# Performance work log

Measured on AMD Instinct MI355X. Metric: run time of the kernel, lower is better.

The kernel has to match this reference:

```python
import jax, jax.numpy as jnp
import numpy as np

HID = 128  # args['hidden_size']


def preprocess_adj(A):
    # A: [B, N, N] -> D^{-1/2} (A + I) D^{-1/2}
    N = A.shape[1]
    A_hat = A + jnp.eye(N, dtype=A.dtype)
    d = jnp.sum(A_hat, axis=2)                     # [B, N]
    d_safe = jnp.where(d > 0, d, 1.0)
    d_inv = jnp.where(d > 0, d_safe ** -0.5, 0.0)  # inf -> 0, as in torch code
    return d_inv[:, :, None] * A_hat * d_inv[:, None, :]


def lstm(x, w_ih, w_hh, b_ih, b_hh):
    # x: [B, T, H]; PyTorch gate order i, f, g, o; zero init state
    B = x.shape[0]
    H = w_hh.shape[1]
    def step(carry, xt):
        h, c = carry
        z = xt @ w_ih.T + b_ih + h @ w_hh.T + b_hh
        i, f, g, o = jnp.split(z, 4, axis=-1)
        c = jax.nn.sigmoid(f) * c + jax.nn.sigmoid(i) * jnp.tanh(g)
        h = jax.nn.sigmoid(o) * jnp.tanh(c)
        return (h, c), h
    h0 = jnp.zeros((B, H), x.dtype)
    c0 = jnp.zeros((B, H), x.dtype)
    _, hs = jax.lax.scan(step, (h0, c0), jnp.swapaxes(x, 0, 1))
    return jnp.swapaxes(hs, 0, 1)  # [B, T, H]


def gcn_dynamic_forward(x, A_norm, conv_w, conv_b, w_ih, w_hh, b_ih, b_hh):
    # x: [B, N, HID] with N >= HID: take last HID rows as dynamic-filter input
    df_in = x[:, x.shape[1] - HID:, :]              # [B, HID, HID]
    dyn = jax.lax.conv_general_dilated(
        df_in, conv_w, window_strides=(1,), padding=[(1, 1)],
        dimension_numbers=('NCH', 'OIH', 'NCH')) + conv_b[None, :, None]
    lw = lstm(dyn, w_ih, w_hh, b_ih, b_hh)          # [B, HID, HID]
    agg = jnp.matmul(A_norm, x)                     # [B, N, HID]
    out = jax.nn.sigmoid(jnp.matmul(agg, lw))       # output activation (1-layer GCN)
    return out                                       # dropout is identity in eval


def setup_inputs() -> dict:
    key = jax.random.key(0)
    ks = jax.random.split(key, 8)
    B, N = 4, 4096
    node_embedding = jax.random.normal(ks[0], (B, N, HID), dtype=jnp.float32)
    # sparse symmetric-ish 0/1 adjacency, avg degree ~ N*0.01
    adjacency_matrix = (jax.random.uniform(ks[1], (B, N, N)) < 0.01).astype(jnp.float32)
    s = 0.05
    conv_w = jax.random.normal(ks[2], (HID, HID, 3), dtype=jnp.float32) * s
    conv_b = jax.random.normal(ks[3], (HID,), dtype=jnp.float32) * s
    w_ih = jax.random.normal(ks[4], (4 * HID, HID), dtype=jnp.float32) * s
    w_hh = jax.random.normal(ks[5], (4 * HID, HID), dtype=jnp.float32) * s
    b_ih = jax.random.normal(ks[6], (4 * HID,), dtype=jnp.float32) * s
    b_hh = jax.random.normal(ks[7], (4 * HID,), dtype=jnp.float32) * s
    return {"node_embedding": node_embedding, "adjacency_matrix": adjacency_matrix,
            "conv_w": conv_w, "conv_b": conv_b,
            "w_ih": w_ih, "w_hh": w_hh, "b_ih": b_ih, "b_hh": b_hh}


def reference(node_embedding, adjacency_matrix, conv_w, conv_b, w_ih, w_hh, b_ih, b_hh):
    A_norm = preprocess_adj(adjacency_matrix)
    return gcn_dynamic_forward(node_embedding, A_norm, conv_w, conv_b, w_ih, w_hh, b_ih, b_hh)
```

## Files before the change

### kernel.cpp

```cpp
#include <hip/hip_runtime.h>
#include <hip/hip_cooperative_groups.h>
#include <math.h>

namespace cg = cooperative_groups;

#define N_NODES 4096
#define HIDN 128
#define MAXNZ 128
#define CGRID 512
#define NTHR 512

typedef float v4f __attribute__((ext_vector_type(4)));
typedef _Float16 h2 __attribute__((ext_vector_type(2)));
typedef _Float16 h8 __attribute__((ext_vector_type(8)));

__device__ __forceinline__ float fsig(float x) { return 1.0f / (1.0f + __expf(-x)); }
__device__ __forceinline__ float ftanh_(float x) { return 1.0f - 2.0f / (__expf(2.0f * x) + 1.0f); }


__device__ __forceinline__ void convz_body(
        int cb, int tid, const float* __restrict__ x,
        const float* __restrict__ conv_w, const float* __restrict__ conv_b,
        const float* __restrict__ w_ih, const float* __restrict__ b_ih,
        const float* __restrict__ b_hh, float* __restrict__ z3,
        float* dl ) {
    const int b = cb >> 5;
    const int t0 = (cb & 31) * 4;
    const int tsub = tid >> 7;
    const int h = tid & 127;
    const int t = t0 + tsub;
    {
        const float* xb = x + ((size_t)b * N_NODES + (N_NODES - HIDN)) * HIDN;
        const float* w = conv_w + (size_t)t * HIDN * 3;
        float a0 = conv_b[t], a1 = 0.0f, a2 = 0.0f, a3 = 0.0f;
        #pragma unroll 4
        for (int i = 0; i < HIDN; i += 4) {
            const float* xr0 = xb + (size_t)i * HIDN;
            #pragma unroll
            for (int s = 0; s < 4; ++s) {
                const float* xr = xr0 + s * HIDN;
                float w0 = w[(i + s) * 3 + 0], w1 = w[(i + s) * 3 + 1], w2 = w[(i + s) * 3 + 2];
                float left  = (h > 0)   ? xr[h - 1] : 0.0f;
                float mid   = xr[h];
                float right = (h < 127) ? xr[h + 1] : 0.0f;
                if (s == 0)      a0 += left * w0 + mid * w1 + right * w2;
                else if (s == 1) a1 += left * w0 + mid * w1 + right * w2;
                else if (s == 2) a2 += left * w0 + mid * w1 + right * w2;
                else             a3 += left * w0 + mid * w1 + right * w2;
            }
        }
        dl[tsub * HIDN + h] = (a0 + a1) + (a2 + a3);
    }
    __syncthreads();
    const int u = tid;
    const int qg = u >> 7;
    const int m  = u & 127;
    const float4* wr = (const float4*)(w_ih + (size_t)u * HIDN);
    float bias = b_ih[u] + b_hh[u];
    float acc0 = bias, acc1 = bias, acc2 = bias, acc3 = bias;
    #pragma unroll
    for (int half = 0; half < 2; ++half) {
        float4 wv[16];
        #pragma unroll
        for (int j = 0; j < 16; ++j) wv[j] = wr[half * 16 + j];
        const float4* d0 = (const float4*)(dl + 0 * HIDN) + half * 16;
        const float4* d1 = (const float4*)(dl + 1 * HIDN) + half * 16;
        const float4* d2 = (const float4*)(dl + 2 * HIDN) + half * 16;
        const float4* d3 = (const float4*)(dl + 3 * HIDN) + half * 16;
        #pragma unroll
        for (int j = 0; j < 16; ++j) {
            float4 wj = wv[j];
            float4 v0 = d0[j], v1 = d1[j], v2 = d2[j], v3 = d3[j];
            acc0 += wj.x * v0.x + wj.y * v0.y + wj.z * v0.z + wj.w * v0.w;
            acc1 += wj.x * v1.x + wj.y * v1.y + wj.z * v1.z + wj.w * v1.w;
            acc2 += wj.x * v2.x + wj.y * v2.y + wj.z * v2.z + wj.w * v2.w;
            acc3 += wj.x * v3.x + wj.y * v3.y + wj.z * v3.z + wj.w * v3.w;
        }
    }
    float* zb = z3 + (size_t)b * HIDN * HIDN * 4;
    zb[((size_t)(t0 + 0) * 128 + m) * 4 + qg] = acc0;
    zb[((size_t)(t0 + 1) * 128 + m) * 4 + qg] = acc1;
    zb[((size_t)(t0 + 2) * 128 + m) * 4 + qg] = acc2;
    zb[((size_t)(t0 + 3) * 128 + m) * 4 + qg] = acc3;
}

__device__ __forceinline__ void ascan_row(
        int r, int lane, const float* __restrict__ A, float* __restrict__ d_inv,
        int* __restrict__ cnt, int* __restrict__ idx, int* sidx_w) {
    const v4f* row = (const v4f*)(A + (size_t)r * N_NODES);
    const unsigned long long below = (1ull << lane) - 1ull;
    int cbase = 0;
    v4f cur[4], nxt[4];
    #pragma unroll
    for (int j = 0; j < 4; ++j) cur[j] = row[j * 64 + lane];
#define PROC1(c, col)                                                         \
    {                                                                         \
        bool nz = ((c) != 0.0f);                                              \
        unsigned long long mm = __ballot(nz);                                 \
        if (mm) {                                                             \
            if (nz) {                                                         \
                int p_ = cbase + __popcll(mm & below);                        \
                if (p_ < MAXNZ) sidx_w[p_] = (col);                           \
            }                                                                 \
            cbase += __popcll(mm);                                            \
        }                                                                     \
    }
    #pragma unroll
    for (int g = 0; g < 4; ++g) {
        if (g < 3) {
            #pragma unroll
            for (int j = 0; j < 4; ++j) nxt[j] = row[(g + 1) * 256 + j * 64 + lane];
        }
        #pragma unroll
        for (int j = 0; j < 4; ++j) {
            int col0 = ((g * 4 + j) * 64 + lane) * 4;
            PROC1(cur[j].x, col0 + 0);
            PROC1(cur[j].y, col0 + 1);
            PROC1(cur[j].z, col0 + 2);
            PROC1(cur[j].w, col0 + 3);
        }
        #pragma unroll
        for (int j = 0; j < 4; ++j) cur[j] = nxt[j];
    }
#undef PROC1
    int cnt_r = (cbase < MAXNZ) ? cbase : MAXNZ;
    for (int k = lane; k < cnt_r; k += 64)
        idx[r * MAXNZ + k] = sidx_w[k];
    if (lane == 0) {
        cnt[r] = cnt_r;
        d_inv[r] = rsqrtf((float)(cbase + 1));
    }
}

__device__ __forceinline__ void lstm_body(
        int b, int t, const float* __restrict__ z3, const float* __restrict__ w_hh,
        float* __restrict__ lw, float4* zl, _Float16* hb) {
    const int m = t >> 2;
    const int q = t & 3;
    h2 w2[4][16];
    #pragma unroll
    for (int g = 0; g < 4; ++g) {
        const float4* wr = (const float4*)(w_hh + ((size_t)(g * HIDN + m)) * HIDN + q * 32);
        #pragma unroll
        for (int j4 = 0; j4 < 8; ++j4) {
            float4 wv = wr[j4];
            w2[g][2 * j4 + 0] = h2{(_Float16)wv.x, (_Float16)wv.y};
            w2[g][2 * j4 + 1] = h2{(_Float16)wv.z, (_Float16)wv.w};
        }
    }
    float c = 0.0f;
    if (t < 64) ((h2*)hb)[t] = h2{(_Float16)0.0f, (_Float16)0.0f};
    const float4* zsrc = (const float4*)z3 + (size_t)b * 16384;
    float* lwb = lw + (size_t)b * HIDN * HIDN + m;
    float hist[4];
    for (int ch = 0; ch < 8; ++ch) {
        const float4* src = zsrc + ch * 2048;
        #pragma unroll
        for (int k = 0; k < 4; ++k)
            zl[t + 512 * k] = src[t + 512 * k];
        __syncthreads();
        #pragma unroll
        for (int si = 0; si < 16; ++si) {
            const int s = ch * 16 + si;
            const h8* hp = ((const h8*)(hb + (size_t)(s & 1) * HIDN)) + q * 4;
            h8 H0 = hp[0], H1 = hp[1], H2 = hp[2], H3 = hp[3];
            float4 zv = zl[si * 128 + m];
            float a0 = 0.f, a1 = 0.f, a2 = 0.f, a3 = 0.f;
            #pragma unroll
            for (int j = 0; j < 16; ++j) {
                h2 hj = (j < 4)  ? ((const h2*)&H0)[j]
                      : (j < 8)  ? ((const h2*)&H1)[j - 4]
                      : (j < 12) ? ((const h2*)&H2)[j - 8]
                                 : ((const h2*)&H3)[j - 12];
                a0 = __builtin_amdgcn_fdot2(w2[0][j], hj, a0, false);
                a1 = __builtin_amdgcn_fdot2(w2[1][j], hj, a1, false);
                a2 = __builtin_amdgcn_fdot2(w2[2][j], hj, a2, false);
                a3 = __builtin_amdgcn_fdot2(w2[3][j], hj, a3, false);
            }
            a0 += __shfl_xor(a0, 1); a0 += __shfl_xor(a0, 2);
            a1 += __shfl_xor(a1, 1); a1 += __shfl_xor(a1, 2);
            a2 += __shfl_xor(a2, 1); a2 += __shfl_xor(a2, 2);
            a3 += __shfl_xor(a3, 1); a3 += __shfl_xor(a3, 2);
            float zi = a0 + zv.x;
            float zf = a1 + zv.y;
            float zg = a2 + zv.z;
            float zo = a3 + zv.w;
            float ig = fsig(zi);
            float fg = fsig(zf);
            float gg = ftanh_(zg);
            float og = fsig(zo);
            c = fg * c + ig * gg;
            float hn = og * ftanh_(c);
            if (q == (si & 3)) hist[si >> 2] = hn;
            if (q == 0) hb[(size_t)((s + 1) & 1) * HIDN + m] = (_Float16)hn;
            __syncthreads();
        }
        #pragma unroll
        for (int j = 0; j < 4; ++j)
            lwb[(size_t)(ch * 16 + q + 4 * j) * HIDN] = hist[j];
    }
}

__device__ __forceinline__ void gather_row(
        int r, int lane, const float* __restrict__ x,
        const float* __restrict__ d_inv, const int* __restrict__ cnt,
        const int* __restrict__ idx, float* __restrict__ agg) {
    const int b = r >> 12;
    const int i = r & 4095;
    const float* dv = d_inv + (b << 12);
    const float2* xb = (const float2*)(x + (size_t)b * N_NODES * HIDN);
    const int* irow = idx + r * MAXNZ;
    const int n = cnt[r];
    float ax = 0.0f, ay = 0.0f;
    int k = 0;
    for (; k + 8 <= n; k += 8) {
        int4 j0 = *(const int4*)&irow[k];
        int4 j1 = *(const int4*)&irow[k + 4];
        float2 v0 = xb[(size_t)j0.x * 64 + lane];
        float2 v1 = xb[(size_t)j0.y * 64 + lane];
        float2 v2 = xb[(size_t)j0.z * 64 + lane];
        float2 v3 = xb[(size_t)j0.w * 64 + lane];
        float2 v4 = xb[(size_t)j1.x * 64 + lane];
        float2 v5 = xb[(size_t)j1.y * 64 + lane];
        float2 v6 = xb[(size_t)j1.z * 64 + lane];
        float2 v7 = xb[(size_t)j1.w * 64 + lane];
        float d0 = dv[j0.x], d1 = dv[j0.y], d2 = dv[j0.z], d3 = dv[j0.w];
        float d4 = dv[j1.x], d5 = dv[j1.y], d6 = dv[j1.z], d7 = dv[j1.w];
        ax += d0 * v0.x + d1 * v1.x + d2 * v2.x + d3 * v3.x
            + d4 * v4.x + d5 * v5.x + d6 * v6.x + d7 * v7.x;
        ay += d0 * v0.y + d1 * v1.y + d2 * v2.y + d3 * v3.y
            + d4 * v4.y + d5 * v5.y + d6 * v6.y + d7 * v7.y;
    }
    for (; k < n; ++k) {
        int j = irow[k];
        float dj = dv[j];
        float2 v = xb[(size_t)j * 64 + lane];
        ax += dj * v.x;
        ay += dj * v.y;
    }
    float di = dv[i];
    float2 vi = xb[(size_t)i * 64 + lane];
    float2 o2;
    o2.x = di * (ax + di * vi.x);
    o2.y = di * (ay + di * vi.y);
    ((float2*)(agg + (size_t)r * HIDN))[lane] = o2;
}

__device__ __forceinline__ void outmm_body(
        int bb, int tid, const float* __restrict__ agg,
        const float* __restrict__ lw, float* __restrict__ out, float* lw_lds) {
    const int i0 = bb * 32;
    const int b = i0 >> 12;
    const float4* lwg = (const float4*)(lw + (size_t)b * HIDN * HIDN);
    float4* lds4 = (float4*)lw_lds;
    for (int v = tid; v < HIDN * HIDN / 4; v += NTHR) lds4[v] = lwg[v];
    __syncthreads();
    const int r0 = i0 + (tid >> 4);
    const int u0 = (tid & 15) * 4;
    const float4* a4 = (const float4*)agg;
    float4 acc[2];
    acc[0] = make_float4(0.f, 0.f, 0.f, 0.f);
    acc[1] = make_float4(0.f, 0.f, 0.f, 0.f);
    for (int f4 = 0; f4 < 32; ++f4) {
        float4 a0 = a4[(size_t)r0 * 32 + f4];
        #pragma unroll
        for (int ff = 0; ff < 4; ++ff) {
            float af0 = (ff == 0) ? a0.x : (ff == 1) ? a0.y : (ff == 2) ? a0.z : a0.w;
            const float* wrow = lw_lds + (f4 * 4 + ff) * HIDN + u0;
            #pragma unroll
            for (int cc = 0; cc < 2; ++cc) {
                float4 wv = *(const float4*)(wrow + cc * 64);
                acc[cc].x += af0 * wv.x; acc[cc].y += af0 * wv.y;
                acc[cc].z += af0 * wv.z; acc[cc].w += af0 * wv.w;
            }
        }
    }
    #pragma unroll
    for (int cc = 0; cc < 2; ++cc) {
        float4 ov;
        ov.x = fsig(acc[cc].x);
        ov.y = fsig(acc[cc].y);
        ov.z = fsig(acc[cc].z);
        ov.w = fsig(acc[cc].w);
        *(float4*)(out + (size_t)r0 * HIDN + u0 + cc * 64) = ov;
    }
}

__global__ __launch_bounds__(NTHR)
__attribute__((amdgpu_waves_per_eu(4, 4)))
void k_fused(
        const float* __restrict__ x, const float* __restrict__ A,
        const float* __restrict__ conv_w, const float* __restrict__ conv_b,
        const float* __restrict__ w_ih, const float* __restrict__ w_hh,
        const float* __restrict__ b_ih, const float* __restrict__ b_hh,
        float* __restrict__ z3, float* __restrict__ d_inv,
        int* __restrict__ cnt, int* __restrict__ idx,
        float* __restrict__ lw, float* __restrict__ agg,
        float* __restrict__ out) {
    __shared__ __align__(16) char arena[65536];
    cg::grid_group grid = cg::this_grid();
    const int tid = threadIdx.x;
    const int bid = blockIdx.x;
    const int wid = tid >> 6;
    const int lane = tid & 63;

    if (bid < 128) {
        convz_body(bid, tid, x, conv_w, conv_b, w_ih, b_ih, b_hh, z3, (float*)arena);
    } else {
        int* sidx_w = (int*)arena + wid * MAXNZ;
        const int gw = (bid - 128) * 8 + wid;
        for (int r = gw; r < 16384; r += 3072)
            ascan_row(r, lane, A, d_inv, cnt, idx, sidx_w);
    }
    __threadfence();
    grid.sync();

    if (bid < 4) {
        lstm_body(bid, tid, z3, w_hh, lw, (float4*)arena, (_Float16*)(arena + 32768));
    } else {
        const int gw = (bid - 4) * 8 + wid;
        for (int r = gw; r < 16384; r += 4064)
            gather_row(r, lane, x, d_inv, cnt, idx, agg);
    }
    __threadfence();
    grid.sync();

    outmm_body(bid, tid, agg, lw, out, (float*)arena);
}

__global__ __launch_bounds__(512) void k1_fb(
        const float* __restrict__ x, const float* __restrict__ conv_w,
        const float* __restrict__ conv_b, const float* __restrict__ w_ih,
        const float* __restrict__ b_ih, const float* __restrict__ b_hh,
        float* __restrict__ z3,
        const float* __restrict__ A, float* __restrict__ d_inv,
        int* __restrict__ cnt, int* __restrict__ idx) {
    __shared__ __align__(16) char arena[4096];
    if (blockIdx.x < 128) {
        convz_body(blockIdx.x, threadIdx.x, x, conv_w, conv_b, w_ih, b_ih, b_hh,
                   z3, (float*)arena);
    } else {
        const int wid = threadIdx.x >> 6;
        const int lane = threadIdx.x & 63;
        int* sidx_w = (int*)arena + wid * MAXNZ;
        ascan_row((blockIdx.x - 128) * 8 + wid, lane, A, d_inv, cnt, idx, sidx_w);
    }
}

__global__ __launch_bounds__(512)
__attribute__((amdgpu_waves_per_eu(4, 4)))
void k2_fb(
        const float* __restrict__ z3, const float* __restrict__ w_hh,
        float* __restrict__ lw,
        const float* __restrict__ x, const float* __restrict__ d_inv,
        const int* __restrict__ cnt, const int* __restrict__ idx,
        float* __restrict__ agg) {
    __shared__ __align__(16) char arena[33280];
    if (blockIdx.x < 4) {
        lstm_body(blockIdx.x, threadIdx.x, z3, w_hh, lw,
                  (float4*)arena, (_Float16*)(arena + 32768));
    } else {
        const int wid = threadIdx.x >> 6;
        const int lane = threadIdx.x & 63;
        gather_row((blockIdx.x - 4) * 8 + wid, lane, x, d_inv, cnt, idx, agg);
    }
}

__global__ __launch_bounds__(512) void k3_fb(
        const float* __restrict__ agg, const float* __restrict__ lw,
        float* __restrict__ out) {
    __shared__ __align__(16) char arena[65536];
    outmm_body(blockIdx.x, threadIdx.x, agg, lw, out, (float*)arena);
}

extern "C" void kernel_launch(void* const* d_in, const int* in_sizes, int n_in,
                              void* d_out, int out_size, void* d_ws, size_t ws_size,
                              hipStream_t stream) {
    const float* x      = (const float*)d_in[0];
    const float* A      = (const float*)d_in[1];
    const float* conv_w = (const float*)d_in[2];
    const float* conv_b = (const float*)d_in[3];
    const float* w_ih   = (const float*)d_in[4];
    const float* w_hh   = (const float*)d_in[5];
    const float* b_ih   = (const float*)d_in[6];
    const float* b_hh   = (const float*)d_in[7];
    float* out = (float*)d_out;

    char* ws = (char*)d_ws;
    float* d_inv = (float*)ws;
    int*   cnt   = (int*)(ws + 65536);
    int*   idx   = (int*)(ws + 131072);
    float* z3    = (float*)(ws + 131072 + 8388608);
    float* lw    = (float*)(ws + 131072 + 8388608 + 1048576);
    float* agg   = (float*)(ws + 131072 + 8388608 + 1048576 + 262144);

    static int coop_ok = -1;
    if (coop_ok < 0) {
        int nb = 0;
        hipError_t qerr = hipOccupancyMaxActiveBlocksPerMultiprocessor(
            &nb, (const void*)k_fused, NTHR, 0);
        coop_ok = (qerr == hipSuccess && nb * 256 >= CGRID) ? 1 : 0;
    }

    if (coop_ok == 1) {
        void* args[] = {
            (void*)&x, (void*)&A, (void*)&conv_w, (void*)&conv_b,
            (void*)&w_ih, (void*)&w_hh, (void*)&b_ih, (void*)&b_hh,
            (void*)&z3, (void*)&d_inv, (void*)&cnt, (void*)&idx,
            (void*)&lw, (void*)&agg, (void*)&out,
        };
        hipError_t err = hipLaunchCooperativeKernel(
            (const void*)k_fused, dim3(CGRID), dim3(NTHR), (void**)args, 0, stream);
        if (err == hipSuccess) return;
        coop_ok = 0;
    }

    hipLaunchKernelGGL(k1_fb, dim3(2176), dim3(512), 0, stream,
                       x, conv_w, conv_b, w_ih, b_ih, b_hh, z3, A, d_inv, cnt, idx);
    hipLaunchKernelGGL(k2_fb, dim3(2052), dim3(512), 0, stream,
                       z3, w_hh, lw, x, d_inv, cnt, idx, agg);
    hipLaunchKernelGGL(k3_fb, dim3(512), dim3(512), 0, stream, agg, lw, out);
}
```

Baseline: 500.6 us.

## Use 1024-thread blocks with half the cooperative grid, splitting LSTM dot across eight lanes

Doubles the block size to 1024 threads and halves the cooperative grid to 256 blocks, so there is one block per CU. The work mapping is rewritten for each phase: the conv/z stage handles 8 timesteps per block, scan and gather use 16 waves per block, and the output matmul takes 64 rows per block. The serial LSTM recurrence now spreads each hidden unit's dot product over 8 lanes instead of 4, which halves per-thread work and register weights on the critical path but adds one more shuffle-reduction step. Removing the waves_per_eu attribute and using larger blocks changes register pressure and occupancy, and every block-wide sync now has to wait on twice as many threads.

```diff
diff --git a/kernel.cpp b/kernel.cpp
--- a/kernel.cpp
+++ b/kernel.cpp
@@ -7,8 +7,8 @@
 #define N_NODES 4096
 #define HIDN 128
 #define MAXNZ 128
-#define CGRID 512
-#define NTHR 512
+#define CGRID 256
+#define NTHR 1024
 
 typedef float v4f __attribute__((ext_vector_type(4)));
 typedef _Float16 h2 __attribute__((ext_vector_type(2)));
@@ -23,9 +23,9 @@
         const float* __restrict__ conv_w, const float* __restrict__ conv_b,
         const float* __restrict__ w_ih, const float* __restrict__ b_ih,
         const float* __restrict__ b_hh, float* __restrict__ z3,
-        float* dl ) {
-    const int b = cb >> 5;
-    const int t0 = (cb & 31) * 4;
+        float* dl) {
+    const int b = cb >> 4;
+    const int t0 = (cb & 15) * 8;
     const int tsub = tid >> 7;
     const int h = tid & 127;
     const int t = t0 + tsub;
@@ -52,7 +52,8 @@
         dl[tsub * HIDN + h] = (a0 + a1) + (a2 + a3);
     }
     __syncthreads();
-    const int u = tid;
+    const int u = tid & 511;
+    const int tp = tid >> 9;
     const int qg = u >> 7;
     const int m  = u & 127;
     const float4* wr = (const float4*)(w_ih + (size_t)u * HIDN);
@@ -63,10 +64,10 @@
         float4 wv[16];
         #pragma unroll
         for (int j = 0; j < 16; ++j) wv[j] = wr[half * 16 + j];
-        const float4* d0 = (const float4*)(dl + 0 * HIDN) + half * 16;
-        const float4* d1 = (const float4*)(dl + 1 * HIDN) + half * 16;
-        const float4* d2 = (const float4*)(dl + 2 * HIDN) + half * 16;
-        const float4* d3 = (const float4*)(dl + 3 * HIDN) + half * 16;
+        const float4* d0 = (const float4*)(dl + (tp * 4 + 0) * HIDN) + half * 16;
+        const float4* d1 = (const float4*)(dl + (tp * 4 + 1) * HIDN) + half * 16;
+        const float4* d2 = (const float4*)(dl + (tp * 4 + 2) * HIDN) + half * 16;
+        const float4* d3 = (const float4*)(dl + (tp * 4 + 3) * HIDN) + half * 16;
         #pragma unroll
         for (int j = 0; j < 16; ++j) {
             float4 wj = wv[j];
@@ -78,10 +79,11 @@
         }
     }
     float* zb = z3 + (size_t)b * HIDN * HIDN * 4;
-    zb[((size_t)(t0 + 0) * 128 + m) * 4 + qg] = acc0;
-    zb[((size_t)(t0 + 1) * 128 + m) * 4 + qg] = acc1;
-    zb[((size_t)(t0 + 2) * 128 + m) * 4 + qg] = acc2;
-    zb[((size_t)(t0 + 3) * 128 + m) * 4 + qg] = acc3;
+    const int tb = t0 + tp * 4;
+    zb[((size_t)(tb + 0) * 128 + m) * 4 + qg] = acc0;
+    zb[((size_t)(tb + 1) * 128 + m) * 4 + qg] = acc1;
+    zb[((size_t)(tb + 2) * 128 + m) * 4 + qg] = acc2;
+    zb[((size_t)(tb + 3) * 128 + m) * 4 + qg] = acc3;
 }
 
 __device__ __forceinline__ void ascan_row(
@@ -135,14 +137,14 @@
 __device__ __forceinline__ void lstm_body(
         int b, int t, const float* __restrict__ z3, const float* __restrict__ w_hh,
         float* __restrict__ lw, float4* zl, _Float16* hb) {
-    const int m = t >> 2;
-    const int q = t & 3;
-    h2 w2[4][16];
+    const int m = t >> 3;
+    const int q = t & 7;
+    h2 w2[4][8];
     #pragma unroll
     for (int g = 0; g < 4; ++g) {
-        const float4* wr = (const float4*)(w_hh + ((size_t)(g * HIDN + m)) * HIDN + q * 32);
-        #pragma unroll
-        for (int j4 = 0; j4 < 8; ++j4) {
+        const float4* wr = (const float4*)(w_hh + ((size_t)(g * HIDN + m)) * HIDN + q * 16);
+        #pragma unroll
+        for (int j4 = 0; j4 < 4; ++j4) {
             float4 wv = wr[j4];
             w2[g][2 * j4 + 0] = h2{(_Float16)wv.x, (_Float16)wv.y};
             w2[g][2 * j4 + 1] = h2{(_Float16)wv.z, (_Float16)wv.w};
@@ -152,35 +154,31 @@
     if (t < 64) ((h2*)hb)[t] = h2{(_Float16)0.0f, (_Float16)0.0f};
     const float4* zsrc = (const float4*)z3 + (size_t)b * 16384;
     float* lwb = lw + (size_t)b * HIDN * HIDN + m;
-    float hist[4];
+    float hist[2];
     for (int ch = 0; ch < 8; ++ch) {
         const float4* src = zsrc + ch * 2048;
-        #pragma unroll
-        for (int k = 0; k < 4; ++k)
-            zl[t + 512 * k] = src[t + 512 * k];
+        zl[t] = src[t];
+        zl[t + 1024] = src[t + 1024];
         __syncthreads();
         #pragma unroll
         for (int si = 0; si < 16; ++si) {
             const int s = ch * 16 + si;
-            const h8* hp = ((const h8*)(hb + (size_t)(s & 1) * HIDN)) + q * 4;
-            h8 H0 = hp[0], H1 = hp[1], H2 = hp[2], H3 = hp[3];
+            const h8* hp = ((const h8*)(hb + (size_t)(s & 1) * HIDN)) + q * 2;
+            h8 H0 = hp[0], H1 = hp[1];
             float4 zv = zl[si * 128 + m];
             float a0 = 0.f, a1 = 0.f, a2 = 0.f, a3 = 0.f;
             #pragma unroll
-            for (int j = 0; j < 16; ++j) {
-                h2 hj = (j < 4)  ? ((const h2*)&H0)[j]
-                      : (j < 8)  ? ((const h2*)&H1)[j - 4]
-                      : (j < 12) ? ((const h2*)&H2)[j - 8]
-                                 : ((const h2*)&H3)[j - 12];
+            for (int j = 0; j < 8; ++j) {
+                h2 hj = (j < 4) ? ((const h2*)&H0)[j] : ((const h2*)&H1)[j - 4];
                 a0 = __builtin_amdgcn_fdot2(w2[0][j], hj, a0, false);
                 a1 = __builtin_amdgcn_fdot2(w2[1][j], hj, a1, false);
                 a2 = __builtin_amdgcn_fdot2(w2[2][j], hj, a2, false);
                 a3 = __builtin_amdgcn_fdot2(w2[3][j], hj, a3, false);
             }
-            a0 += __shfl_xor(a0, 1); a0 += __shfl_xor(a0, 2);
-            a1 += __shfl_xor(a1, 1); a1 += __shfl_xor(a1, 2);
-            a2 += __shfl_xor(a2, 1); a2 += __shfl_xor(a2, 2);
-            a3 += __shfl_xor(a3, 1); a3 += __shfl_xor(a3, 2);
+            a0 += __shfl_xor(a0, 1); a0 += __shfl_xor(a0, 2); a0 += __shfl_xor(a0, 4);
+            a1 += __shfl_xor(a1, 1); a1 += __shfl_xor(a1, 2); a1 += __shfl_xor(a1, 4);
+            a2 += __shfl_xor(a2, 1); a2 += __shfl_xor(a2, 2); a2 += __shfl_xor(a2, 4);
+            a3 += __shfl_xor(a3, 1); a3 += __shfl_xor(a3, 2); a3 += __shfl_xor(a3, 4);
             float zi = a0 + zv.x;
             float zf = a1 + zv.y;
             float zg = a2 + zv.z;
@@ -191,13 +189,12 @@
             float og = fsig(zo);
             c = fg * c + ig * gg;
             float hn = og * ftanh_(c);
-            if (q == (si & 3)) hist[si >> 2] = hn;
+            if (q == (si & 7)) hist[si >> 3] = hn;
             if (q == 0) hb[(size_t)((s + 1) & 1) * HIDN + m] = (_Float16)hn;
             __syncthreads();
         }
-        #pragma unroll
-        for (int j = 0; j < 4; ++j)
-            lwb[(size_t)(ch * 16 + q + 4 * j) * HIDN] = hist[j];
+        lwb[(size_t)(ch * 16 + q) * HIDN]     = hist[0];
+        lwb[(size_t)(ch * 16 + q + 8) * HIDN] = hist[1];
     }
 }
 
@@ -249,7 +246,7 @@
 __device__ __forceinline__ void outmm_body(
         int bb, int tid, const float* __restrict__ agg,
         const float* __restrict__ lw, float* __restrict__ out, float* lw_lds) {
-    const int i0 = bb * 32;
+    const int i0 = bb * 64;
     const int b = i0 >> 12;
     const float4* lwg = (const float4*)(lw + (size_t)b * HIDN * HIDN);
     float4* lds4 = (float4*)lw_lds;
@@ -286,9 +283,7 @@
     }
 }
 
-__global__ __launch_bounds__(NTHR)
-__attribute__((amdgpu_waves_per_eu(4, 4)))
-void k_fused(
+__global__ __launch_bounds__(NTHR) void k_fused(
         const float* __restrict__ x, const float* __restrict__ A,
         const float* __restrict__ conv_w, const float* __restrict__ conv_b,
         const float* __restrict__ w_ih, const float* __restrict__ w_hh,
@@ -304,11 +299,11 @@
     const int wid = tid >> 6;
     const int lane = tid & 63;
 
-    if (bid < 128) {
+    if (bid < 64) {
         convz_body(bid, tid, x, conv_w, conv_b, w_ih, b_ih, b_hh, z3, (float*)arena);
     } else {
         int* sidx_w = (int*)arena + wid * MAXNZ;
-        const int gw = (bid - 128) * 8 + wid;
+        const int gw = (bid - 64) * 16 + wid;
         for (int r = gw; r < 16384; r += 3072)
             ascan_row(r, lane, A, d_inv, cnt, idx, sidx_w);
     }
@@ -318,8 +313,8 @@
     if (bid < 4) {
         lstm_body(bid, tid, z3, w_hh, lw, (float4*)arena, (_Float16*)(arena + 32768));
     } else {
-        const int gw = (bid - 4) * 8 + wid;
-        for (int r = gw; r < 16384; r += 4064)
+        const int gw = (bid - 4) * 16 + wid;
+        for (int r = gw; r < 16384; r += 4032)
             gather_row(r, lane, x, d_inv, cnt, idx, agg);
     }
     __threadfence();
@@ -328,28 +323,28 @@
     outmm_body(bid, tid, agg, lw, out, (float*)arena);
 }
 
-__global__ __launch_bounds__(512) void k1_fb(
+__global__ __launch_bounds__(NTHR) void k1_fb(
         const float* __restrict__ x, const float* __restrict__ conv_w,
         const float* __restrict__ conv_b, const float* __restrict__ w_ih,
         const float* __restrict__ b_ih, const float* __restrict__ b_hh,
         float* __restrict__ z3,
         const float* __restrict__ A, float* __restrict__ d_inv,
         int* __restrict__ cnt, int* __restrict__ idx) {
-    __shared__ __align__(16) char arena[4096];
-    if (blockIdx.x < 128) {
+    __shared__ __align__(16) char arena[8192];
+    if (blockIdx.x < 64) {
         convz_body(blockIdx.x, threadIdx.x, x, conv_w, conv_b, w_ih, b_ih, b_hh,
                    z3, (float*)arena);
     } else {
         const int wid = threadIdx.x >> 6;
         const int lane = threadIdx.x & 63;
         int* sidx_w = (int*)arena + wid * MAXNZ;
-        ascan_row((blockIdx.x - 128) * 8 + wid, lane, A, d_inv, cnt, idx, sidx_w);
-    }
-}
-
-__global__ __launch_bounds__(512)
-__attribute__((amdgpu_waves_per_eu(4, 4)))
-void k2_fb(
+        const int gw = ((int)blockIdx.x - 64) * 16 + wid;
+        for (int r = gw; r < 16384; r += 3072)
+            ascan_row(r, lane, A, d_inv, cnt, idx, sidx_w);
+    }
+}
+
+__global__ __launch_bounds__(NTHR) void k2_fb(
         const float* __restrict__ z3, const float* __restrict__ w_hh,
         float* __restrict__ lw,
         const float* __restrict__ x, const float* __restrict__ d_inv,
@@ -362,11 +357,13 @@
     } else {
         const int wid = threadIdx.x >> 6;
         const int lane = threadIdx.x & 63;
-        gather_row((blockIdx.x - 4) * 8 + wid, lane, x, d_inv, cnt, idx, agg);
-    }
-}
-
-__global__ __launch_bounds__(512) void k3_fb(
+        const int gw = ((int)blockIdx.x - 4) * 16 + wid;
+        for (int r = gw; r < 16384; r += 4032)
+            gather_row(r, lane, x, d_inv, cnt, idx, agg);
+    }
+}
+
+__global__ __launch_bounds__(NTHR) void k3_fb(
         const float* __restrict__ agg, const float* __restrict__ lw,
         float* __restrict__ out) {
     __shared__ __align__(16) char arena[65536];
@@ -415,9 +412,9 @@
         coop_ok = 0;
     }
 
-    hipLaunchKernelGGL(k1_fb, dim3(2176), dim3(512), 0, stream,
+    hipLaunchKernelGGL(k1_fb, dim3(256), dim3(NTHR), 0, stream,
                        x, conv_w, conv_b, w_ih, b_ih, b_hh, z3, A, d_inv, cnt, idx);
-    hipLaunchKernelGGL(k2_fb, dim3(2052), dim3(512), 0, stream,
+    hipLaunchKernelGGL(k2_fb, dim3(256), dim3(NTHR), 0, stream,
                        z3, w_hh, lw, x, d_inv, cnt, idx, agg);
-    hipLaunchKernelGGL(k3_fb, dim3(512), dim3(512), 0, stream, agg, lw, out);
-}
+    hipLaunchKernelGGL(k3_fb, dim3(256), dim3(NTHR), 0, stream, agg, lw, out);
+}
```

Measured after the change: 557.9 us. +11.5%, slower.
